# Kernel optimization log

Measured on AMD Instinct MI355X. Metric: run time of the kernel, lower is better.

## Reference

```python
import jax, jax.numpy as jnp
import numpy as np

N_NODES = 200000
N_EDGES = 6400000
A_TOPO, A_PARAM, A_KCL, A_KVL, A_SPARSE = 1.0, 1.0, 0.1, 0.1, 0.01
EPS = 1e-6


def setup_inputs() -> dict:
    key = jax.random.key(0)
    k = jax.random.split(key, 7)
    # voltages near 1.0 p.u. (cols 0,1), loads small (cols 2,3)
    node_features = jnp.concatenate([
        1.0 + 0.05 * jax.random.normal(k[0], (N_NODES, 2), dtype=jnp.float32),
        0.1 * jax.random.normal(k[1], (N_NODES, 2), dtype=jnp.float32),
    ], axis=1)
    edge_index = jax.random.randint(k[2], (2, N_EDGES), 0, N_NODES)
    edge_logits = jax.random.normal(k[3], (N_EDGES,), dtype=jnp.float32)
    # R,X kept away from zero so 1/(R+eps) stays finite-scale
    edge_params = 0.1 + 0.5 * jax.random.uniform(k[4], (N_EDGES, 2), dtype=jnp.float32)
    edge_labels = (jax.random.uniform(k[5], (N_EDGES,)) < 0.5).astype(jnp.float32)
    target_edge_params = 0.1 + 0.5 * jax.random.uniform(k[6], (N_EDGES, 2), dtype=jnp.float32)
    return dict(node_features=node_features, edge_logits=edge_logits,
                edge_params=edge_params, edge_labels=edge_labels,
                target_edge_params=target_edge_params, edge_index=edge_index)


def _segsum(x, ids, n):
    return jax.ops.segment_sum(x, ids, num_segments=n)


def reference(node_features, edge_logits, edge_params, edge_labels,
              target_edge_params, edge_index):
    N = node_features.shape[0]
    src, dst = edge_index[0], edge_index[1]
    probs = jax.nn.sigmoid(edge_logits)                      # [E]
    R, X = edge_params[:, 0], edge_params[:, 1]

    # ---- topology: BCEWithLogits (mean) ----
    bce = -(edge_labels * jax.nn.log_sigmoid(edge_logits)
            + (1.0 - edge_labels) * jax.nn.log_sigmoid(-edge_logits))
    topology = A_TOPO * jnp.mean(bce)

    # ---- parameter: MSE ----
    parameter = A_PARAM * jnp.mean((edge_params - target_edge_params) ** 2)

    # ---- KCL: per-edge |I| = |v_src - v_dst| / |Z + 1e-6| (1e-6 added to real part) ----
    dvr = node_features[src, 0] - node_features[dst, 0]      # [E]
    dvi = node_features[src, 1] - node_features[dst, 1]
    cur = jnp.sqrt(dvr * dvr + dvi * dvi) / jnp.sqrt((R + EPS) ** 2 + X * X)
    curp = cur * probs
    # node sum: -|I|p at src, +|I|p at dst (self-loops cancel, same as original)
    node_cur = _segsum(curp, dst, N) - _segsum(curp, src, N)  # [N]
    kcl = A_KCL * jnp.mean(node_cur ** 2)

    # ---- KVL: parameter consistency + voltage-drop variance ----
    w = probs[:, None]                                       # [E,1]
    mean_params = (edge_params * w).sum(axis=0) / (probs.sum() + EPS)  # [2]
    param_var = (((edge_params - mean_params) ** 2) * w).sum(axis=0)   # [2]
    param_consistency = param_var.mean()
    vdrop = jnp.sqrt(dvr * dvr + dvi * dvi) * probs          # [E]
    voltage_consistency = jnp.var(vdrop, ddof=1)             # torch.var unbiased
    kvl = A_KVL * (param_consistency + voltage_consistency)

    # ---- radiality (weighted 0.1 in main loss) ----
    edge_count_loss = (probs.sum() - (N - 1)) ** 2
    radial = 0.1 * (1.0 * edge_count_loss + 0.1 * probs.mean())

    # ---- sparsity ----
    sparsity = A_SPARSE * probs.mean()

    return jnp.stack([topology, parameter, kcl, kvl, radial, sparsity,
                      topology + parameter + kcl + kvl + radial + sparsity])
```

## Files before the change

### kernel.cpp

```cpp
#include <hip/hip_runtime.h>


constexpr int   kNodes         = 200000;
constexpr int   kEdges         = 6400000;
constexpr int   kNumSums       = 9;
constexpr float kEps           = 1e-6f;

constexpr int   kBucketShift   = 12;
constexpr int   kBucketSize    = 1 << kBucketShift;
constexpr int   kBuckets       = (kNodes + kBucketSize - 1) / kBucketSize;
constexpr int   kEdgesPerBlk   = 1024;
constexpr int   kEdgesPerThr   = 4;
constexpr int   kEntPerThr     = 8;
constexpr int   kP1Blocks      = kEdges / kEdgesPerBlk;
static_assert(kEdges % kEdgesPerBlk == 0, "exact tiling assumed");
constexpr int   kEntriesPerBlk = 2 * kEdgesPerBlk;
constexpr int   kOffStride     = 52;
constexpr int   kSlabs         = 16;
constexpr int   kBlocksPerSlab = (kP1Blocks + kSlabs - 1) / kSlabs;
constexpr int   kP2Blocks      = kBuckets * kSlabs;
constexpr int   kNodeBlocks    = 256;
constexpr int   kFbBlocks      = 2048;
constexpr float kQScale        = 65536.0f;
constexpr float kQInv          = 1.0f / 65536.0f;
constexpr int   kQBias         = 524288;

__device__ __forceinline__ float softplusf(float t) {
    return fmaxf(t, 0.0f) + log1pf(expf(-fabsf(t)));
}

__global__ __launch_bounds__(256) void compact_nf(
    const float4* __restrict__ nf4,
    float2*       __restrict__ nfc)
{
    const int i = blockIdx.x * 256 + threadIdx.x;
    if (i < kNodes) {
        const float4 v = nf4[i];
        nfc[i] = make_float2(v.x, v.y);
    }
}

__global__ __launch_bounds__(256) void p1_edges(
    const float2* __restrict__ nfc,
    const float*  __restrict__ logits,
    const float*  __restrict__ eparams,
    const float*  __restrict__ labels,
    const float*  __restrict__ tparams,
    const int*    __restrict__ srcs,
    const int*    __restrict__ dsts,
    unsigned*       __restrict__ pairs,
    unsigned short* __restrict__ offs_g,
    float*          __restrict__ partials)
{
    __shared__ unsigned sorted[kEntriesPerBlk];
    __shared__ int   hist[kBuckets];
    __shared__ int   offs[kBuckets + 1];
    __shared__ int   cursor[kBuckets];
    __shared__ float smem[4][kNumSums];

    const int tid = threadIdx.x;
    for (int b = tid; b < kBuckets; b += 256) hist[b] = 0;
    __syncthreads();

    float acc[kNumSums];
#pragma unroll
    for (int k = 0; k < kNumSums; ++k) acc[k] = 0.0f;

    unsigned ent[kEntPerThr];
    unsigned bkp[2];

    const int e0 = blockIdx.x * kEdgesPerBlk;
    const int q4 = (e0 >> 2) + tid;

    const int4 ss = reinterpret_cast<const int4*>(srcs)[q4];
    const int4 dd = reinterpret_cast<const int4*>(dsts)[q4];

    const float2 vs0 = nfc[ss.x];
    const float2 vs1 = nfc[ss.y];
    const float2 vs2 = nfc[ss.z];
    const float2 vs3 = nfc[ss.w];
    const float2 vd0 = nfc[dd.x];
    const float2 vd1 = nfc[dd.y];
    const float2 vd2 = nfc[dd.z];
    const float2 vd3 = nfc[dd.w];

    const float4 lx = reinterpret_cast<const float4*>(logits)[q4];
    const float4 ly = reinterpret_cast<const float4*>(labels)[q4];
    const float4 ea = reinterpret_cast<const float4*>(eparams)[2 * q4];
    const float4 eb = reinterpret_cast<const float4*>(eparams)[2 * q4 + 1];
    const float4 ta = reinterpret_cast<const float4*>(tparams)[2 * q4];
    const float4 tb = reinterpret_cast<const float4*>(tparams)[2 * q4 + 1];

    const float xs[4]  = {lx.x, lx.y, lx.z, lx.w};
    const float ys[4]  = {ly.x, ly.y, ly.z, ly.w};
    const float epr[4] = {ea.x, ea.z, eb.x, eb.z};
    const float epx[4] = {ea.y, ea.w, eb.y, eb.w};
    const float tpr[4] = {ta.x, ta.z, tb.x, tb.z};
    const float tpx[4] = {ta.y, ta.w, tb.y, tb.w};
    const float2 vss[4] = {vs0, vs1, vs2, vs3};
    const float2 vdd[4] = {vd0, vd1, vd2, vd3};
    const int    sn[4]  = {ss.x, ss.y, ss.z, ss.w};
    const int    dn[4]  = {dd.x, dd.y, dd.z, dd.w};

    unsigned bp0 = 0, bp1 = 0;
#pragma unroll
    for (int j = 0; j < kEdgesPerThr; ++j) {
        const float x = xs[j], y = ys[j];
        const float er = epr[j], ex = epx[j];

        const float t      = __expf(-fabsf(x));
        const float inv1pt = __builtin_amdgcn_rcpf(1.0f + t);
        const float p      = (x >= 0.0f) ? inv1pt : t * inv1pt;
        const float sp_nx  = fmaxf(-x, 0.0f) + __logf(1.0f + t);
        const float bce    = sp_nx + (1.0f - y) * x;

        const float dr  = er - tpr[j];
        const float dxx = ex - tpx[j];

        const float dvr = vss[j].x - vdd[j].x;
        const float dvi = vss[j].y - vdd[j].y;
        const float mag = sqrtf(dvr * dvr + dvi * dvi);

        const float Rp    = er + kEps;
        const float curp  = mag * rsqrtf(Rp * Rp + ex * ex) * p;
        const float vdrop = mag * p;

        acc[0] += bce;
        acc[1] += dr * dr + dxx * dxx;
        acc[2] += p;
        acc[3] += p * er;
        acc[4] += p * ex;
        acc[5] += p * er * er;
        acc[6] += p * ex * ex;
        acc[7] += vdrop;
        acc[8] += vdrop * vdrop;

        int q = __float2int_rn(curp * kQScale);
        q = max(-(kQBias - 1), min(kQBias - 1, q));

        const int bd = dn[j] >> kBucketShift;
        const int bs = sn[j] >> kBucketShift;
        atomicAdd(&hist[bd], 1);
        atomicAdd(&hist[bs], 1);

        ent[2 * j]     = ((unsigned)(dn[j] & (kBucketSize - 1)) << 20) | (unsigned)( q + kQBias);
        ent[2 * j + 1] = ((unsigned)(sn[j] & (kBucketSize - 1)) << 20) | (unsigned)(-q + kQBias);
        if (j < 2) {
            bp0 |= ((unsigned)bd) << (16 * j);
            bp0 |= ((unsigned)bs) << (16 * j + 8);
        } else {
            bp1 |= ((unsigned)bd) << (16 * (j - 2));
            bp1 |= ((unsigned)bs) << (16 * (j - 2) + 8);
        }
    }
    bkp[0] = bp0;
    bkp[1] = bp1;
    __syncthreads();

    if (tid < 64) {
        const int lane = tid;
        int h    = (lane < kBuckets) ? hist[lane] : 0;
        int incl = h;
#pragma unroll
        for (int o = 1; o < 64; o <<= 1) {
            int n = __shfl_up(incl, o, 64);
            if (lane >= o) incl += n;
        }
        if (lane < kBuckets) {
            offs[lane]   = incl - h;
            cursor[lane] = 0;
        }
        if (lane == 0) offs[kBuckets] = kEntriesPerBlk;
    }
    __syncthreads();

#pragma unroll
    for (int k = 0; k < kEntPerThr; ++k) {
        const int b   = (int)((bkp[k >> 2] >> ((k & 3) * 8)) & 0xFFu);
        const int pos = offs[b] + atomicAdd(&cursor[b], 1);
        sorted[pos] = ent[k];
    }
    __syncthreads();

    unsigned* pout = pairs + (size_t)blockIdx.x * kEntriesPerBlk;
    for (int j = tid; j < kEntriesPerBlk; j += 256)
        pout[j] = sorted[j];
    if (tid < kBuckets + 1)
        offs_g[(size_t)blockIdx.x * kOffStride + tid] = (unsigned short)offs[tid];

    const int lane = tid & 63;
    const int wave = tid >> 6;
#pragma unroll
    for (int k = 0; k < kNumSums; ++k) {
        float v = acc[k];
#pragma unroll
        for (int off = 32; off > 0; off >>= 1) v += __shfl_down(v, off, 64);
        if (lane == 0) smem[wave][k] = v;
    }
    __syncthreads();
    if (tid < kNumSums) {
        float v = 0.0f;
#pragma unroll
        for (int w = 0; w < 4; ++w) v += smem[w][tid];
        partials[blockIdx.x * kNumSums + tid] = v;
    }
}

__global__ __launch_bounds__(256) void p2_buckets(
    const unsigned*       __restrict__ pairs,
    const unsigned short* __restrict__ offs_g,
    int*                  __restrict__ out_i32)
{
    __shared__ int accs[kBucketSize];
    const int b    = blockIdx.x / kSlabs;
    const int slab = blockIdx.x % kSlabs;

    for (int i = threadIdx.x; i < kBucketSize; i += 256) accs[i] = 0;
    __syncthreads();

    const int i0 = slab * kBlocksPerSlab;
    const int i1 = min(i0 + kBlocksPerSlab, kP1Blocks);
    const int lane = threadIdx.x & 63;
    const int wave = threadIdx.x >> 6;

    for (int i = i0 + wave; i < i1; i += 4) {
        const int o0 = (int)offs_g[(size_t)i * kOffStride + b];
        const int o1 = (int)offs_g[(size_t)i * kOffStride + b + 1];
        const unsigned* pb = pairs + (size_t)i * kEntriesPerBlk;
        for (int j = o0 + lane; j < o1; j += 64) {
            const unsigned u = pb[j];
            atomicAdd(&accs[u >> 20], (int)(u & 0xFFFFFu) - kQBias);
        }
    }
    __syncthreads();

    int* o = out_i32 + (size_t)blockIdx.x * kBucketSize;
    for (int i = threadIdx.x; i < kBucketSize; i += 256) o[i] = accs[i];
}

__global__ __launch_bounds__(256) void node_pass_binned(
    const int* __restrict__ out_i32,
    float*     __restrict__ node_partials)
{
    float acc = 0.0f;
    const int stride = gridDim.x * blockDim.x;
    for (int n = blockIdx.x * blockDim.x + threadIdx.x; n < kNodes; n += stride) {
        const int b = n >> kBucketShift;
        const int s = n & (kBucketSize - 1);
        const int* p = out_i32 + ((size_t)b * kSlabs) * kBucketSize + s;
        int v = 0;
#pragma unroll
        for (int m = 0; m < kSlabs; ++m) v += p[(size_t)m * kBucketSize];
        const float nc = (float)v * kQInv;
        acc += nc * nc;
    }
    __shared__ float smem[4];
    const int lane = threadIdx.x & 63;
    const int wave = threadIdx.x >> 6;
    float v = acc;
#pragma unroll
    for (int off = 32; off > 0; off >>= 1) v += __shfl_down(v, off, 64);
    if (lane == 0) smem[wave] = v;
    __syncthreads();
    if (threadIdx.x == 0)
        node_partials[blockIdx.x] = smem[0] + smem[1] + smem[2] + smem[3];
}

__global__ __launch_bounds__(256) void edge_pass_atomic(
    const float* __restrict__ nf, const float* __restrict__ logits,
    const float* __restrict__ eparams, const float* __restrict__ labels,
    const float* __restrict__ tparams, const int* __restrict__ srcs,
    const int* __restrict__ dsts, float* __restrict__ node_cur,
    float* __restrict__ partials)
{
    float acc[kNumSums];
#pragma unroll
    for (int k = 0; k < kNumSums; ++k) acc[k] = 0.0f;
    const int stride = gridDim.x * blockDim.x;
    for (int e = blockIdx.x * blockDim.x + threadIdx.x; e < kEdges; e += stride) {
        float  x  = logits[e];
        float  y  = labels[e];
        float2 ep = *reinterpret_cast<const float2*>(eparams + 2 * e);
        float2 tp = *reinterpret_cast<const float2*>(tparams + 2 * e);
        int    s  = srcs[e];
        int    d  = dsts[e];
        float2 vs = *reinterpret_cast<const float2*>(nf + 4 * s);
        float2 vd = *reinterpret_cast<const float2*>(nf + 4 * d);
        float p   = 1.0f / (1.0f + expf(-x));
        float bce = y * softplusf(-x) + (1.0f - y) * softplusf(x);
        float dr = ep.x - tp.x, dxx = ep.y - tp.y;
        float dvr = vs.x - vd.x, dvi = vs.y - vd.y;
        float mag = sqrtf(dvr * dvr + dvi * dvi);
        float Rp  = ep.x + kEps;
        float den = sqrtf(Rp * Rp + ep.y * ep.y);
        float curp = (mag / den) * p;
        float vdrop = mag * p;
        acc[0] += bce; acc[1] += dr * dr + dxx * dxx; acc[2] += p;
        acc[3] += p * ep.x; acc[4] += p * ep.y;
        acc[5] += p * ep.x * ep.x; acc[6] += p * ep.y * ep.y;
        acc[7] += vdrop; acc[8] += vdrop * vdrop;
        atomicAdd(node_cur + d,  curp);
        atomicAdd(node_cur + s, -curp);
    }
    __shared__ float smem[4][kNumSums];
    const int lane = threadIdx.x & 63, wave = threadIdx.x >> 6;
#pragma unroll
    for (int k = 0; k < kNumSums; ++k) {
        float v = acc[k];
#pragma unroll
        for (int off = 32; off > 0; off >>= 1) v += __shfl_down(v, off, 64);
        if (lane == 0) smem[wave][k] = v;
    }
    __syncthreads();
    if (threadIdx.x < kNumSums) {
        float v = 0.0f;
#pragma unroll
        for (int w = 0; w < 4; ++w) v += smem[w][threadIdx.x];
        partials[blockIdx.x * kNumSums + threadIdx.x] = v;
    }
}

__global__ __launch_bounds__(256) void node_pass_flat(
    const float* __restrict__ node_cur, float* __restrict__ node_partials)
{
    float acc = 0.0f;
    const int stride = gridDim.x * blockDim.x;
    for (int i = blockIdx.x * blockDim.x + threadIdx.x; i < kNodes; i += stride) {
        float v = node_cur[i];
        acc += v * v;
    }
    __shared__ float smem[4];
    const int lane = threadIdx.x & 63, wave = threadIdx.x >> 6;
    float v = acc;
#pragma unroll
    for (int off = 32; off > 0; off >>= 1) v += __shfl_down(v, off, 64);
    if (lane == 0) smem[wave] = v;
    __syncthreads();
    if (threadIdx.x == 0)
        node_partials[blockIdx.x] = smem[0] + smem[1] + smem[2] + smem[3];
}

__global__ __launch_bounds__(256) void finalize(
    const float* __restrict__ partials, int nblocks,
    const float* __restrict__ node_partials, int nnp,
    float*       __restrict__ out)
{
    const int tid  = threadIdx.x;
    const int lane = tid & 63;
    const int wave = tid >> 6;
    __shared__ double red[4][kNumSums + 1];

    double s[kNumSums];
#pragma unroll
    for (int k = 0; k < kNumSums; ++k) s[k] = 0.0;
    for (int i = tid; i < nblocks; i += 256) {
#pragma unroll
        for (int k = 0; k < kNumSums; ++k)
            s[k] += (double)partials[i * kNumSums + k];
    }
    double ns = 0.0;
    for (int i = tid; i < nnp; i += 256) ns += (double)node_partials[i];

#pragma unroll
    for (int k = 0; k < kNumSums + 1; ++k) {
        double v = (k < kNumSums) ? s[k] : ns;
#pragma unroll
        for (int off = 32; off > 0; off >>= 1) v += __shfl_down(v, off, 64);
        if (lane == 0) red[wave][k] = v;
    }
    __syncthreads();

    if (tid == 0) {
        double sums[kNumSums + 1];
#pragma unroll
        for (int k = 0; k < kNumSums + 1; ++k)
            sums[k] = red[0][k] + red[1][k] + red[2][k] + red[3][k];

        const double E = (double)kEdges, N = (double)kNodes;
        const double s_bce = sums[0], s_par = sums[1], s_p = sums[2];
        const double s_pR = sums[3], s_pX = sums[4];
        const double s_pR2 = sums[5], s_pX2 = sums[6];
        const double s_v = sums[7], s_v2 = sums[8];
        const double nsum = sums[9];

        double topology  = s_bce / E;
        double parameter = s_par / (2.0 * E);
        double kcl       = 0.1 * (nsum / N);

        double denom = s_p + (double)kEps;
        double mR = s_pR / denom, mX = s_pX / denom;
        double varR = s_pR2 - 2.0 * mR * s_pR + mR * mR * s_p;
        double varX = s_pX2 - 2.0 * mX * s_pX + mX * mX * s_p;
        double param_consistency = 0.5 * (varR + varX);
        double voltage_consistency = (s_v2 - (s_v * s_v) / E) / (E - 1.0);
        double kvl = 0.1 * (param_consistency + voltage_consistency);

        double ecl = s_p - (N - 1.0);
        ecl = ecl * ecl;
        double radial   = 0.1 * (ecl + 0.1 * (s_p / E));
        double sparsity = 0.01 * (s_p / E);
        double total = topology + parameter + kcl + kvl + radial + sparsity;

        out[0] = (float)topology;  out[1] = (float)parameter;
        out[2] = (float)kcl;       out[3] = (float)kvl;
        out[4] = (float)radial;    out[5] = (float)sparsity;
        out[6] = (float)total;
    }
}

extern "C" void kernel_launch(void* const* d_in, const int* in_sizes, int n_in,
                              void* d_out, int out_size, void* d_ws, size_t ws_size,
                              hipStream_t stream) {
    const float* nf      = (const float*)d_in[0];
    const float* logits  = (const float*)d_in[1];
    const float* eparams = (const float*)d_in[2];
    const float* labels  = (const float*)d_in[3];
    const float* tparams = (const float*)d_in[4];
    const int*   eidx    = (const int*)d_in[5];
    float* out           = (float*)d_out;

    const size_t n_pairs  = (size_t)kP1Blocks * kEntriesPerBlk;
    const size_t n_outi32 = (size_t)kP2Blocks * kBucketSize;
    const size_t n_nfc    = (size_t)kNodes * 2;
    const size_t n_offs_w = ((size_t)kP1Blocks * kOffStride + 1) / 2 + 64;
    const size_t n_words  = n_pairs + n_outi32 + n_nfc + n_offs_w +
                            (size_t)kP1Blocks * kNumSums + kNodeBlocks;

    if (ws_size >= n_words * sizeof(unsigned)) {
        unsigned*       pairs         = (unsigned*)d_ws;
        int*            out_i32       = (int*)(pairs + n_pairs);
        float2*         nfc           = (float2*)(out_i32 + n_outi32);
        unsigned short* offs_g        = (unsigned short*)((unsigned*)nfc + n_nfc);
        float*          partials      = (float*)((unsigned*)offs_g + n_offs_w);
        float*          node_partials = partials + (size_t)kP1Blocks * kNumSums;

        compact_nf<<<(kNodes + 255) / 256, 256, 0, stream>>>(
            (const float4*)nf, nfc);
        p1_edges<<<kP1Blocks, 256, 0, stream>>>(nfc, logits, eparams, labels,
                                                tparams, eidx, eidx + kEdges,
                                                pairs, offs_g, partials);
        p2_buckets<<<kP2Blocks, 256, 0, stream>>>(pairs, offs_g, out_i32);
        node_pass_binned<<<kNodeBlocks, 256, 0, stream>>>(out_i32, node_partials);
        finalize<<<1, 256, 0, stream>>>(partials, kP1Blocks, node_partials,
                                        kNodeBlocks, out);
    } else {
        float* node_cur      = (float*)d_ws;
        float* partials      = node_cur + kNodes;
        float* node_partials = partials + (size_t)kFbBlocks * kNumSums;

        hipMemsetAsync(node_cur, 0, kNodes * sizeof(float), stream);
        edge_pass_atomic<<<kFbBlocks, 256, 0, stream>>>(nf, logits, eparams, labels,
                                                        tparams, eidx, eidx + kEdges,
                                                        node_cur, partials);
        node_pass_flat<<<kNodeBlocks, 256, 0, stream>>>(node_cur, node_partials);
        finalize<<<1, 256, 0, stream>>>(partials, kFbBlocks, node_partials,
                                        kNodeBlocks, out);
    }
}
```

Baseline: 167.2 us.

## Tighten binning kernels: vectorized stores, software-prefetched bucket scan, wider p2 blocks

In p1_edges the scan runs in every wave instead of only wave 0, and cursor clearing moves into the initial zeroing. Together these remove one block barrier, and the sorted entries are written out as uint4 vectors. p2_buckets moves to 512 threads and prefetches the next tile's offsets and first entry while it does atomics on the current tile, to hide global load latency. node_pass_binned reads four nodes per thread with int4 loads and uses 200 blocks. Every wave now writes the same offs values redundantly. The offs[kBuckets] slot now comes from the inclusive scan total instead of a constant.

```diff
diff --git a/kernel.cpp b/kernel.cpp
--- a/kernel.cpp
+++ b/kernel.cpp
@@ -11,15 +11,16 @@
 constexpr int   kBuckets       = (kNodes + kBucketSize - 1) / kBucketSize;
 constexpr int   kEdgesPerBlk   = 1024;
 constexpr int   kEdgesPerThr   = 4;
-constexpr int   kEntPerThr     = 8;
 constexpr int   kP1Blocks      = kEdges / kEdgesPerBlk;
 static_assert(kEdges % kEdgesPerBlk == 0, "exact tiling assumed");
 constexpr int   kEntriesPerBlk = 2 * kEdgesPerBlk;
 constexpr int   kOffStride     = 52;
 constexpr int   kSlabs         = 16;
-constexpr int   kBlocksPerSlab = (kP1Blocks + kSlabs - 1) / kSlabs;
+constexpr int   kTilesPerSlab  = (kP1Blocks + kSlabs - 1) / kSlabs;
 constexpr int   kP2Blocks      = kBuckets * kSlabs;
-constexpr int   kNodeBlocks    = 256;
+constexpr int   kP2Threads     = 512;
+constexpr int   kP2Waves       = kP2Threads / 64;
+constexpr int   kNodeBlocks    = 200;
 constexpr int   kFbBlocks      = 2048;
 constexpr float kQScale        = 65536.0f;
 constexpr float kQInv          = 1.0f / 65536.0f;
@@ -52,22 +53,21 @@
     unsigned short* __restrict__ offs_g,
     float*          __restrict__ partials)
 {
-    __shared__ unsigned sorted[kEntriesPerBlk];
+    __shared__ __align__(16) unsigned sorted[kEntriesPerBlk];
     __shared__ int   hist[kBuckets];
     __shared__ int   offs[kBuckets + 1];
     __shared__ int   cursor[kBuckets];
     __shared__ float smem[4][kNumSums];
 
     const int tid = threadIdx.x;
-    for (int b = tid; b < kBuckets; b += 256) hist[b] = 0;
+    if (tid < kBuckets) { hist[tid] = 0; cursor[tid] = 0; }
     __syncthreads();
 
     float acc[kNumSums];
 #pragma unroll
     for (int k = 0; k < kNumSums; ++k) acc[k] = 0.0f;
 
-    unsigned ent[kEntPerThr];
-    unsigned bkp[2];
+    unsigned ent[2 * kEdgesPerThr];
 
     const int e0 = blockIdx.x * kEdgesPerBlk;
     const int q4 = (e0 >> 2) + tid;
@@ -153,12 +153,11 @@
             bp1 |= ((unsigned)bs) << (16 * (j - 2) + 8);
         }
     }
-    bkp[0] = bp0;
-    bkp[1] = bp1;
-    __syncthreads();
-
-    if (tid < 64) {
-        const int lane = tid;
+
+    __syncthreads();
+
+    {
+        const int lane = tid & 63;
         int h    = (lane < kBuckets) ? hist[lane] : 0;
         int incl = h;
 #pragma unroll
@@ -166,25 +165,26 @@
             int n = __shfl_up(incl, o, 64);
             if (lane >= o) incl += n;
         }
-        if (lane < kBuckets) {
-            offs[lane]   = incl - h;
-            cursor[lane] = 0;
+        if (lane < kBuckets + 1) offs[lane] = incl - h;
+    }
+
+    {
+        const unsigned bkp[2] = {bp0, bp1};
+#pragma unroll
+        for (int k = 0; k < 2 * kEdgesPerThr; ++k) {
+            const int b   = (int)((bkp[k >> 2] >> ((k & 3) * 8)) & 0xFFu);
+            const int pos = offs[b] + atomicAdd(&cursor[b], 1);
+            sorted[pos] = ent[k];
         }
-        if (lane == 0) offs[kBuckets] = kEntriesPerBlk;
-    }
-    __syncthreads();
-
-#pragma unroll
-    for (int k = 0; k < kEntPerThr; ++k) {
-        const int b   = (int)((bkp[k >> 2] >> ((k & 3) * 8)) & 0xFFu);
-        const int pos = offs[b] + atomicAdd(&cursor[b], 1);
-        sorted[pos] = ent[k];
-    }
-    __syncthreads();
-
-    unsigned* pout = pairs + (size_t)blockIdx.x * kEntriesPerBlk;
-    for (int j = tid; j < kEntriesPerBlk; j += 256)
-        pout[j] = sorted[j];
+    }
+    __syncthreads();
+
+    {
+        const uint4 v0 = *reinterpret_cast<const uint4*>(&sorted[tid * 4]);
+        reinterpret_cast<uint4*>(pairs + (size_t)blockIdx.x * kEntriesPerBlk)[tid] = v0;
+        const uint4 v1 = *reinterpret_cast<const uint4*>(&sorted[1024 + tid * 4]);
+        reinterpret_cast<uint4*>(pairs + (size_t)blockIdx.x * kEntriesPerBlk)[256 + tid] = v1;
+    }
     if (tid < kBuckets + 1)
         offs_g[(size_t)blockIdx.x * kOffStride + tid] = (unsigned short)offs[tid];
 
@@ -206,7 +206,7 @@
     }
 }
 
-__global__ __launch_bounds__(256) void p2_buckets(
+__global__ __launch_bounds__(kP2Threads) void p2_buckets(
     const unsigned*       __restrict__ pairs,
     const unsigned short* __restrict__ offs_g,
     int*                  __restrict__ out_i32)
@@ -215,27 +215,48 @@
     const int b    = blockIdx.x / kSlabs;
     const int slab = blockIdx.x % kSlabs;
 
-    for (int i = threadIdx.x; i < kBucketSize; i += 256) accs[i] = 0;
-    __syncthreads();
-
-    const int i0 = slab * kBlocksPerSlab;
-    const int i1 = min(i0 + kBlocksPerSlab, kP1Blocks);
+    for (int i = threadIdx.x; i < kBucketSize; i += kP2Threads) accs[i] = 0;
+    __syncthreads();
+
+    const int i0 = slab * kTilesPerSlab;
+    const int i1 = min(i0 + kTilesPerSlab, kP1Blocks);
     const int lane = threadIdx.x & 63;
     const int wave = threadIdx.x >> 6;
 
-    for (int i = i0 + wave; i < i1; i += 4) {
-        const int o0 = (int)offs_g[(size_t)i * kOffStride + b];
-        const int o1 = (int)offs_g[(size_t)i * kOffStride + b + 1];
-        const unsigned* pb = pairs + (size_t)i * kEntriesPerBlk;
-        for (int j = o0 + lane; j < o1; j += 64) {
-            const unsigned u = pb[j];
-            atomicAdd(&accs[u >> 20], (int)(u & 0xFFFFFu) - kQBias);
+    int i = i0 + wave;
+    if (i < i1) {
+        int o0 = (int)offs_g[(size_t)i * kOffStride + b];
+        int o1 = (int)offs_g[(size_t)i * kOffStride + b + 1];
+        unsigned u    = 0;
+        bool     has  = (o0 + lane) < o1;
+        if (has) u = pairs[(size_t)i * kEntriesPerBlk + o0 + lane];
+
+        for (; i < i1; ) {
+            const int ni = i + kP2Waves;
+            int no0 = 0, no1 = 0;
+            unsigned nu = 0;
+            bool nhas = false;
+            if (ni < i1) {
+                no0 = (int)offs_g[(size_t)ni * kOffStride + b];
+                no1 = (int)offs_g[(size_t)ni * kOffStride + b + 1];
+                nhas = (no0 + lane) < no1;
+                if (nhas) nu = pairs[(size_t)ni * kEntriesPerBlk + no0 + lane];
+            }
+
+            if (has) atomicAdd(&accs[u >> 20], (int)(u & 0xFFFFFu) - kQBias);
+            const unsigned* pb = pairs + (size_t)i * kEntriesPerBlk;
+            for (int j = o0 + 64 + lane; j < o1; j += 64) {
+                const unsigned w = pb[j];
+                atomicAdd(&accs[w >> 20], (int)(w & 0xFFFFFu) - kQBias);
+            }
+
+            i = ni; o0 = no0; o1 = no1; u = nu; has = nhas;
         }
     }
     __syncthreads();
 
     int* o = out_i32 + (size_t)blockIdx.x * kBucketSize;
-    for (int i = threadIdx.x; i < kBucketSize; i += 256) o[i] = accs[i];
+    for (int i2 = threadIdx.x; i2 < kBucketSize; i2 += kP2Threads) o[i2] = accs[i2];
 }
 
 __global__ __launch_bounds__(256) void node_pass_binned(
@@ -244,15 +265,22 @@
 {
     float acc = 0.0f;
     const int stride = gridDim.x * blockDim.x;
-    for (int n = blockIdx.x * blockDim.x + threadIdx.x; n < kNodes; n += stride) {
+    for (int n4 = blockIdx.x * blockDim.x + threadIdx.x; n4 < kNodes / 4; n4 += stride) {
+        const int n = n4 * 4;
         const int b = n >> kBucketShift;
         const int s = n & (kBucketSize - 1);
         const int* p = out_i32 + ((size_t)b * kSlabs) * kBucketSize + s;
-        int v = 0;
-#pragma unroll
-        for (int m = 0; m < kSlabs; ++m) v += p[(size_t)m * kBucketSize];
-        const float nc = (float)v * kQInv;
-        acc += nc * nc;
+        int4 v = make_int4(0, 0, 0, 0);
+#pragma unroll
+        for (int m = 0; m < kSlabs; ++m) {
+            const int4 w = *reinterpret_cast<const int4*>(p + (size_t)m * kBucketSize);
+            v.x += w.x; v.y += w.y; v.z += w.z; v.w += w.w;
+        }
+        const float f0 = (float)v.x * kQInv;
+        const float f1 = (float)v.y * kQInv;
+        const float f2 = (float)v.z * kQInv;
+        const float f3 = (float)v.w * kQInv;
+        acc += f0 * f0 + f1 * f1 + f2 * f2 + f3 * f3;
     }
     __shared__ float smem[4];
     const int lane = threadIdx.x & 63;
@@ -439,7 +467,7 @@
         p1_edges<<<kP1Blocks, 256, 0, stream>>>(nfc, logits, eparams, labels,
                                                 tparams, eidx, eidx + kEdges,
                                                 pairs, offs_g, partials);
-        p2_buckets<<<kP2Blocks, 256, 0, stream>>>(pairs, offs_g, out_i32);
+        p2_buckets<<<kP2Blocks, kP2Threads, 0, stream>>>(pairs, offs_g, out_i32);
         node_pass_binned<<<kNodeBlocks, 256, 0, stream>>>(out_i32, node_partials);
         finalize<<<1, 256, 0, stream>>>(partials, kP1Blocks, node_partials,
                                         kNodeBlocks, out);
```

Measured after the change: 136.0 us. 1.23x faster.
